# Optimization experiments

Hardware: AMD Instinct MI355X
Metric: run time of the kernel (lower is better)

The kernel has to match this reference:

```python
import jax, jax.numpy as jnp
import numpy as np

B, S, E, H = 2, 2048, 1280, 20
D = E // H  # head_dim = 64
SCALING = D ** -0.5


def setup_inputs() -> dict:
    key = jax.random.key(0)
    k1, k2, k3, k4, k5 = jax.random.split(key, 5)
    return {
        "hidden_states": jax.random.normal(k1, (B, S, E), dtype=jnp.float32),
        "qkv_w": jax.random.normal(k2, (E, 3 * E), dtype=jnp.float32) * (E ** -0.5),
        "qkv_b": jax.random.normal(k3, (3 * E,), dtype=jnp.float32) * 0.02,
        "out_w": jax.random.normal(k4, (E, E), dtype=jnp.float32) * (E ** -0.5),
        "out_b": jax.random.normal(k5, (E,), dtype=jnp.float32) * 0.02,
    }


def reference(hidden_states, qkv_w, qkv_b, out_w, out_b):
    b, s, e = hidden_states.shape
    # fused QKV projection
    qkv = hidden_states @ qkv_w + qkv_b              # [B,S,3E]
    q, k, v = jnp.split(qkv, 3, axis=-1)
    q = q * SCALING                                  # module pre-scales q; attn uses scaling=1.0
    q = q.reshape(b, s, H, D)
    k = k.reshape(b, s, H, D)
    v = v.reshape(b, s, H, D)
    scores = jnp.einsum("bqhd,bkhd->bhqk", q, k)     # [B,H,S,S]
    # decoder (causal) attention, per AttentionType.DECODER
    causal = jnp.tril(jnp.ones((s, s), dtype=bool))
    scores = jnp.where(causal[None, None], scores, jnp.finfo(scores.dtype).min)
    probs = jax.nn.softmax(scores, axis=-1)
    attn = jnp.einsum("bhqk,bkhd->bqhd", probs, v).reshape(b, s, e)
    return attn @ out_w + out_b
```

## Files before the change

### kernel.cpp

```cpp
#include <hip/hip_runtime.h>
#include <stdint.h>

typedef unsigned short u16;
typedef short s8v __attribute__((ext_vector_type(8)));
typedef float f32x4 __attribute__((ext_vector_type(4)));

#define NB 2
#define NH 20
#define SEQ 2048
#define EMB 1280
#define HD 64
#define MT (NB*SEQ)
#define N3E (3*EMB)
#define QSCALE 0.18033688011112042f

__device__ __forceinline__ u16 f2bf(float f){
  unsigned u = __float_as_uint(f);
  u += 0x7fffu + ((u >> 16) & 1u);
  return (u16)(u >> 16);
}

__global__ void cvt_bf16_kernel(const float* __restrict__ in, u16* __restrict__ out, int n4){
  int i = blockIdx.x*256 + threadIdx.x;
  if (i >= n4) return;
  float4 f = ((const float4* __restrict__)in)[i];
  ushort4 o;
  o.x = f2bf(f.x); o.y = f2bf(f.y); o.z = f2bf(f.z); o.w = f2bf(f.w);
  ((ushort4*)out)[i] = o;
}

__global__ void tconv_kernel(const float* __restrict__ in, u16* __restrict__ out, int R, int C){
  __shared__ float tl[32][33];
  int c0 = blockIdx.x*32, r0 = blockIdx.y*32;
  int tx = threadIdx.x & 31, ty = threadIdx.x >> 5;
  #pragma unroll
  for (int i=0;i<4;i++)
    tl[ty + i*8][tx] = in[(size_t)(r0 + ty + i*8)*C + c0 + tx];
  __syncthreads();
  #pragma unroll
  for (int i=0;i<4;i++)
    out[(size_t)(c0 + ty + i*8)*R + r0 + tx] = f2bf(tl[tx][ty + i*8]);
}

template<int NIT>
__device__ __forceinline__ void stage_swz(const u16* gsrc, int ld, u16* lds, int t){
  #pragma unroll
  for (int i=0;i<NIT;i++){
    int f = i*256 + t;
    int row = f >> 3, sl = f & 7;
    int ssl = sl ^ (row & 7);
    __builtin_amdgcn_global_load_lds(
      (const __attribute__((address_space(1))) void*)(gsrc + (size_t)row*ld + ssl*8),
      (__attribute__((address_space(3))) void*)(lds + f*8), 16, 0, 0);
  }
}

__device__ __forceinline__ s8v frag_ld(const u16* lds, int row, int ks){
  int sl = ks ^ (row & 7);
  return *(const s8v*)(lds + row*64 + sl*8);
}

template<int EPI>
__global__ __launch_bounds__(256) void gemm_bt_kernel(
    const u16* __restrict__ A, const u16* __restrict__ Bt, const float* __restrict__ bias,
    float* __restrict__ Cout, int Ntot, int K,
    u16* __restrict__ qb, u16* __restrict__ kbf, u16* __restrict__ vT)
{
  __shared__ u16 As[128*64];
  __shared__ u16 Bs[128*64];
  int t = threadIdx.x;
  int lane = t & 63, w = t >> 6;
  int wr = w >> 1, wc = w & 1;
  int g = lane >> 4, c = lane & 15;
  int m0 = blockIdx.y*128, n0 = blockIdx.x*128;
  f32x4 acc[4][4] = {};
  for (int k0 = 0; k0 < K; k0 += 64){
    stage_swz<4>(A  + (size_t)m0*K + k0, K, As, t);
    stage_swz<4>(Bt + (size_t)n0*K + k0, K, Bs, t);
    __syncthreads();
    #pragma unroll
    for (int kb2=0;kb2<2;kb2++){
      s8v af[4], bfr[4];
      #pragma unroll
      for (int m=0;m<4;m++) af[m]  = frag_ld(As, wr*64 + m*16 + c, kb2*4 + g);
      #pragma unroll
      for (int n=0;n<4;n++) bfr[n] = frag_ld(Bs, wc*64 + n*16 + c, kb2*4 + g);
      #pragma unroll
      for (int m=0;m<4;m++)
        #pragma unroll
        for (int n=0;n<4;n++)
          acc[m][n] = __builtin_amdgcn_mfma_f32_16x16x32_bf16(af[m], bfr[n], acc[m][n], 0, 0, 0);
    }
    __syncthreads();
  }
  #pragma unroll
  for (int m=0;m<4;m++){
    int growb = m0 + wr*64 + m*16 + g*4;
    #pragma unroll
    for (int n=0;n<4;n++){
      int gcol = n0 + wc*64 + n*16 + c;
      float bv = bias[gcol];
      if (EPI == 1){
        #pragma unroll
        for (int r=0;r<4;r++)
          Cout[(size_t)(growb + r)*Ntot + gcol] = acc[m][n][r] + bv;
      } else {
        int which = gcol / EMB;
        int e = gcol - which*EMB;
        int hh = e >> 6, d = e & 63;
        int bi = growb >> 11, sb = growb & 2047;
        size_t bh = (size_t)bi*NH + hh;
        if (which == 2){
          ushort4 pv;
          pv.x = f2bf(acc[m][n][0] + bv);
          pv.y = f2bf(acc[m][n][1] + bv);
          pv.z = f2bf(acc[m][n][2] + bv);
          pv.w = f2bf(acc[m][n][3] + bv);
          *(ushort4*)(vT + (bh*HD + d)*SEQ + sb) = pv;
        } else {
          u16* dst = (which == 0) ? qb : kbf;
          float scl = (which == 0) ? QSCALE : 1.0f;
          #pragma unroll
          for (int r=0;r<4;r++)
            dst[(bh*SEQ + sb + r)*HD + d] = f2bf((acc[m][n][r] + bv)*scl);
        }
      }
    }
  }
}

__global__ __launch_bounds__(256) void attn_kernel(
    const u16* __restrict__ qb, const u16* __restrict__ kbf, const u16* __restrict__ vT,
    u16* __restrict__ attn)
{
  __shared__ u16 Kls[2][64*64];
  __shared__ u16 Vls[2][64*64];
  __shared__ u16 Ps[4][16*72];
  int bh = blockIdx.x;
  int b = bh / NH, h = bh - b*NH;
  int qt = 31 - blockIdx.y;
  int t = threadIdx.x, lane = t & 63, w = t >> 6;
  int g = lane >> 4, c = lane & 15;
  u16* pw = &Ps[w][0];
  const u16* Kb = kbf + (size_t)bh*SEQ*HD;
  const u16* Vb = vT  + (size_t)bh*HD*SEQ;

  int qwb = qt*64 + w*16;
  const u16* qrow = qb + ((size_t)bh*SEQ + qwb + c)*HD;
  s8v aq0 = *(const s8v*)(qrow + g*8);
  s8v aq1 = *(const s8v*)(qrow + 32 + g*8);
  f32x4 po[4] = {};
  float mrow = -1e30f, lrow = 0.f;

  stage_swz<2>(Kb, HD, Kls[0], t);
  stage_swz<2>(Vb, SEQ, Vls[0], t);

  for (int kt = 0; kt <= qt; ++kt){
    int cur = kt & 1;
    const u16* Ks = Kls[cur];
    const u16* Vs = Vls[cur];
    if (kt < qt){
      int k1 = (kt + 1)*64;
      stage_swz<2>(Kb + (size_t)k1*HD, HD,  Kls[cur^1], t);
      stage_swz<2>(Vb + k1,            SEQ, Vls[cur^1], t);
      asm volatile("s_waitcnt vmcnt(4)" ::: "memory");
    } else {
      asm volatile("s_waitcnt vmcnt(0)" ::: "memory");
    }
    __builtin_amdgcn_s_barrier();
    __builtin_amdgcn_sched_barrier(0);

    int k0 = kt*64;
    s8v vv[8];
    #pragma unroll
    for (int kb2=0;kb2<2;kb2++)
      #pragma unroll
      for (int dt=0;dt<4;dt++)
        vv[kb2*4+dt] = frag_ld(Vs, dt*16 + c, kb2*4 + g);
    f32x4 sc[4];
    #pragma unroll
    for (int nt=0;nt<4;nt++){
      s8v k0f = frag_ld(Ks, nt*16 + c, g);
      s8v k1f = frag_ld(Ks, nt*16 + c, 4 + g);
      f32x4 z = {0.f,0.f,0.f,0.f};
      sc[nt] = __builtin_amdgcn_mfma_f32_16x16x32_bf16(k0f, aq0, z,      0,0,0);
      sc[nt] = __builtin_amdgcn_mfma_f32_16x16x32_bf16(k1f, aq1, sc[nt], 0,0,0);
    }
    if (kt == qt){
      #pragma unroll
      for (int nt=0;nt<4;nt++){
        int kg = k0 + nt*16 + g*4;
        #pragma unroll
        for (int r=0;r<4;r++)
          if (kg + r > qwb + c) sc[nt][r] = -1e30f;
      }
    }
    float mt = fmaxf(fmaxf(sc[0][0],sc[0][1]), fmaxf(sc[0][2],sc[0][3]));
    #pragma unroll
    for (int nt=1;nt<4;nt++)
      mt = fmaxf(mt, fmaxf(fmaxf(sc[nt][0],sc[nt][1]), fmaxf(sc[nt][2],sc[nt][3])));
    mt = fmaxf(mt, __shfl_xor(mt, 16));
    mt = fmaxf(mt, __shfl_xor(mt, 32));
    float mn = fmaxf(mrow, mt);
    float alpha = exp2f(mrow - mn);
    mrow = mn;
    float rs = 0.f;
    #pragma unroll
    for (int nt=0;nt<4;nt++)
      #pragma unroll
      for (int r=0;r<4;r++){
        float pe = exp2f(sc[nt][r] - mn);
        sc[nt][r] = pe;
        rs += pe;
      }
    rs += __shfl_xor(rs, 16);
    rs += __shfl_xor(rs, 32);
    lrow = lrow*alpha + rs;
    float alB[4];
    #pragma unroll
    for (int r=0;r<4;r++)
      alB[r] = __shfl(alpha, (lane & 48) | (g*4 + r));
    #pragma unroll
    for (int dt=0;dt<4;dt++)
      #pragma unroll
      for (int r=0;r<4;r++)
        po[dt][r] *= alB[r];
    #pragma unroll
    for (int nt=0;nt<4;nt++){
      ushort4 pk;
      pk.x = f2bf(sc[nt][0]); pk.y = f2bf(sc[nt][1]);
      pk.z = f2bf(sc[nt][2]); pk.w = f2bf(sc[nt][3]);
      *(ushort4*)(pw + c*72 + nt*16 + g*4) = pk;
    }
    #pragma unroll
    for (int kb2=0;kb2<2;kb2++){
      s8v pa = *(const s8v*)(pw + c*72 + kb2*32 + g*8);
      #pragma unroll
      for (int dt=0;dt<4;dt++)
        po[dt] = __builtin_amdgcn_mfma_f32_16x16x32_bf16(pa, vv[kb2*4+dt], po[dt], 0,0,0);
    }
    asm volatile("s_waitcnt lgkmcnt(0)" ::: "memory");
    __builtin_amdgcn_s_barrier();
  }
  float inv = 1.0f / lrow;
  float invB[4];
  #pragma unroll
  for (int r=0;r<4;r++)
    invB[r] = __shfl(inv, (lane & 48) | (g*4 + r));
  #pragma unroll
  for (int dt=0;dt<4;dt++){
    #pragma unroll
    for (int r=0;r<4;r++){
      int qa = qwb + g*4 + r;
      attn[((size_t)(b*SEQ + qa))*EMB + h*HD + dt*16 + c] = f2bf(po[dt][r] * invB[r]);
    }
  }
}

extern "C" void kernel_launch(void* const* d_in, const int* in_sizes, int n_in,
                              void* d_out, int out_size, void* d_ws, size_t ws_size,
                              hipStream_t stream) {
  const float* hs    = (const float*)d_in[0];
  const float* qkv_w = (const float*)d_in[1];
  const float* qkv_b = (const float*)d_in[2];
  const float* out_w = (const float*)d_in[3];
  const float* out_b = (const float*)d_in[4];
  float* out = (float*)d_out;

  char* p = (char*)d_ws;
  u16* xb    = (u16*)p; p += (size_t)MT*EMB*2;
  u16* wqkvT = (u16*)p; p += (size_t)N3E*EMB*2;
  u16* woT   = (u16*)p; p += (size_t)EMB*EMB*2;
  u16* qbuf  = (u16*)p; p += (size_t)NB*NH*SEQ*HD*2;
  u16* kbuf  = (u16*)p; p += (size_t)NB*NH*SEQ*HD*2;
  u16* vTb   = (u16*)p; p += (size_t)NB*NH*SEQ*HD*2;
  u16* attnb = (u16*)p; p += (size_t)MT*EMB*2;

  cvt_bf16_kernel<<<(MT*EMB/4 + 255)/256, 256, 0, stream>>>(hs, xb, MT*EMB/4);
  tconv_kernel<<<dim3(N3E/32, EMB/32), 256, 0, stream>>>(qkv_w, wqkvT, EMB, N3E);
  tconv_kernel<<<dim3(EMB/32, EMB/32), 256, 0, stream>>>(out_w, woT, EMB, EMB);
  gemm_bt_kernel<0><<<dim3(N3E/128, MT/128), 256, 0, stream>>>(
      xb, wqkvT, qkv_b, nullptr, N3E, EMB, qbuf, kbuf, vTb);
  attn_kernel<<<dim3(40, 32), 256, 0, stream>>>(qbuf, kbuf, vTb, attnb);
  gemm_bt_kernel<1><<<dim3(EMB/128, MT/128), 256, 0, stream>>>(
      attnb, woT, out_b, out, EMB, EMB, nullptr, nullptr, nullptr);
}
```

Measured before the change: 259.5 us.

## Merge prep kernels, add MFMA priority hints, and skip small softmax rescales

```diff
diff --git a/kernel.cpp b/kernel.cpp
--- a/kernel.cpp
+++ b/kernel.cpp
@@ -20,18 +20,30 @@
   return (u16)(u >> 16);
 }
 
-__global__ void cvt_bf16_kernel(const float* __restrict__ in, u16* __restrict__ out, int n4){
-  int i = blockIdx.x*256 + threadIdx.x;
-  if (i >= n4) return;
-  float4 f = ((const float4* __restrict__)in)[i];
-  ushort4 o;
-  o.x = f2bf(f.x); o.y = f2bf(f.y); o.z = f2bf(f.z); o.w = f2bf(f.w);
-  ((ushort4*)out)[i] = o;
-}
-
-__global__ void tconv_kernel(const float* __restrict__ in, u16* __restrict__ out, int R, int C){
+__global__ __launch_bounds__(256) void prep_kernel(
+    const float* __restrict__ hs, const float* __restrict__ qkv_w,
+    const float* __restrict__ out_w,
+    u16* __restrict__ xb, u16* __restrict__ wqkvT, u16* __restrict__ woT)
+{
   __shared__ float tl[32][33];
-  int c0 = blockIdx.x*32, r0 = blockIdx.y*32;
+  int blk = blockIdx.x;
+  if (blk < 5120){
+    int i = blk*256 + threadIdx.x;
+    float4 f = ((const float4* __restrict__)hs)[i];
+    ushort4 o;
+    o.x = f2bf(f.x); o.y = f2bf(f.y); o.z = f2bf(f.z); o.w = f2bf(f.w);
+    ((ushort4*)xb)[i] = o;
+    return;
+  }
+  const float* in; u16* out; int R, C, bx, by;
+  if (blk < 9920){
+    int b2 = blk - 5120; bx = b2 % 120; by = b2 / 120;
+    in = qkv_w; out = wqkvT; R = EMB; C = N3E;
+  } else {
+    int b2 = blk - 9920; bx = b2 % 40; by = b2 / 40;
+    in = out_w; out = woT; R = EMB; C = EMB;
+  }
+  int c0 = bx*32, r0 = by*32;
   int tx = threadIdx.x & 31, ty = threadIdx.x >> 5;
   #pragma unroll
   for (int i=0;i<4;i++)
@@ -178,6 +190,7 @@
       for (int dt=0;dt<4;dt++)
         vv[kb2*4+dt] = frag_ld(Vs, dt*16 + c, kb2*4 + g);
     f32x4 sc[4];
+    __builtin_amdgcn_s_setprio(1);
     #pragma unroll
     for (int nt=0;nt<4;nt++){
       s8v k0f = frag_ld(Ks, nt*16 + c, g);
@@ -186,6 +199,7 @@
       sc[nt] = __builtin_amdgcn_mfma_f32_16x16x32_bf16(k0f, aq0, z,      0,0,0);
       sc[nt] = __builtin_amdgcn_mfma_f32_16x16x32_bf16(k1f, aq1, sc[nt], 0,0,0);
     }
+    __builtin_amdgcn_s_setprio(0);
     if (kt == qt){
       #pragma unroll
       for (int nt=0;nt<4;nt++){
@@ -201,30 +215,33 @@
       mt = fmaxf(mt, fmaxf(fmaxf(sc[nt][0],sc[nt][1]), fmaxf(sc[nt][2],sc[nt][3])));
     mt = fmaxf(mt, __shfl_xor(mt, 16));
     mt = fmaxf(mt, __shfl_xor(mt, 32));
-    float mn = fmaxf(mrow, mt);
-    float alpha = exp2f(mrow - mn);
-    mrow = mn;
+    if (!__all(mt - mrow <= 8.0f)){
+      float mn = fmaxf(mrow, mt);
+      float alpha = exp2f(mrow - mn);
+      mrow = mn;
+      lrow *= alpha;
+      float alB[4];
+      #pragma unroll
+      for (int r=0;r<4;r++)
+        alB[r] = __shfl(alpha, (lane & 48) | (g*4 + r));
+      #pragma unroll
+      for (int dt=0;dt<4;dt++)
+        #pragma unroll
+        for (int r=0;r<4;r++)
+          po[dt][r] *= alB[r];
+    }
     float rs = 0.f;
     #pragma unroll
     for (int nt=0;nt<4;nt++)
       #pragma unroll
       for (int r=0;r<4;r++){
-        float pe = exp2f(sc[nt][r] - mn);
+        float pe = exp2f(sc[nt][r] - mrow);
         sc[nt][r] = pe;
         rs += pe;
       }
     rs += __shfl_xor(rs, 16);
     rs += __shfl_xor(rs, 32);
-    lrow = lrow*alpha + rs;
-    float alB[4];
-    #pragma unroll
-    for (int r=0;r<4;r++)
-      alB[r] = __shfl(alpha, (lane & 48) | (g*4 + r));
-    #pragma unroll
-    for (int dt=0;dt<4;dt++)
-      #pragma unroll
-      for (int r=0;r<4;r++)
-        po[dt][r] *= alB[r];
+    lrow += rs;
     #pragma unroll
     for (int nt=0;nt<4;nt++){
       ushort4 pk;
@@ -232,6 +249,7 @@
       pk.z = f2bf(sc[nt][2]); pk.w = f2bf(sc[nt][3]);
       *(ushort4*)(pw + c*72 + nt*16 + g*4) = pk;
     }
+    __builtin_amdgcn_s_setprio(1);
     #pragma unroll
     for (int kb2=0;kb2<2;kb2++){
       s8v pa = *(const s8v*)(pw + c*72 + kb2*32 + g*8);
@@ -239,6 +257,7 @@
       for (int dt=0;dt<4;dt++)
         po[dt] = __builtin_amdgcn_mfma_f32_16x16x32_bf16(pa, vv[kb2*4+dt], po[dt], 0,0,0);
     }
+    __builtin_amdgcn_s_setprio(0);
     asm volatile("s_waitcnt lgkmcnt(0)" ::: "memory");
     __builtin_amdgcn_s_barrier();
   }
@@ -276,9 +295,7 @@
   u16* vTb   = (u16*)p; p += (size_t)NB*NH*SEQ*HD*2;
   u16* attnb = (u16*)p; p += (size_t)MT*EMB*2;
 
-  cvt_bf16_kernel<<<(MT*EMB/4 + 255)/256, 256, 0, stream>>>(hs, xb, MT*EMB/4);
-  tconv_kernel<<<dim3(N3E/32, EMB/32), 256, 0, stream>>>(qkv_w, wqkvT, EMB, N3E);
-  tconv_kernel<<<dim3(EMB/32, EMB/32), 256, 0, stream>>>(out_w, woT, EMB, EMB);
+  prep_kernel<<<11520, 256, 0, stream>>>(hs, qkv_w, out_w, xb, wqkvT, woT);
   gemm_bt_kernel<0><<<dim3(N3E/128, MT/128), 256, 0, stream>>>(
       xb, wqkvT, qkv_b, nullptr, N3E, EMB, qbuf, kbuf, vTb);
   attn_kernel<<<dim3(40, 32), 256, 0, stream>>>(qbuf, kbuf, vTb, attnb);
```

Measured after the change: 254.3 us. 2.0% less time.
